# Performance work log

Hardware: AMD Instinct MI355X
Metric: run time of the kernel (lower is better)

## Reference

```python
import jax, jax.numpy as jnp
import numpy as np


def _ccl_8(mask):
    """Connected-component labeling with 8-connectivity (skimage connectivity=2).

    Iterative min-label propagation over the 8-neighborhood, accelerated with
    pointer jumping (label compression), run to convergence via lax.while_loop.
    Returns int32 labels: 0 for background, root_pixel_index+1 for each
    component (equivalent to skimage's labels up to a relabeling permutation).
    """
    H, W = mask.shape
    N = H * W
    BIG = jnp.int32(N)  # background sentinel, also maps to itself in the flat table
    idx = jnp.arange(N, dtype=jnp.int32).reshape(H, W)
    init = jnp.where(mask, idx, BIG)

    def neighbor_min(lab):
        # min over self + 8 neighbors, padded with the BIG sentinel
        p = jnp.pad(lab, 1, constant_values=N)
        m = lab
        for dy in (0, 1, 2):
            for dx in (0, 1, 2):
                m = jnp.minimum(m, p[dy:dy + H, dx:dx + W])
        return jnp.where(mask, m, BIG)

    sentinel = jnp.full((1,), N, dtype=jnp.int32)

    def body(state):
        lab, _ = state
        new = neighbor_min(lab)
        # pointer jumping: hop labels through the label table twice (hop doubling)
        for _ in range(2):
            flat = jnp.concatenate([new.reshape(-1), sentinel])  # [N+1]
            new = flat[new]
        return new, jnp.any(new != lab)

    def cond(state):
        return state[1]

    lab, _ = jax.lax.while_loop(cond, body, (init, jnp.array(True)))
    return jnp.where(mask, lab + 1, 0).astype(jnp.int32)


def setup_inputs() -> dict:
    key = jax.random.key(0)
    prob = jax.random.uniform(key, (1, 1, 2048, 2048), dtype=jnp.float32)
    return {"prob": prob}


def reference(prob):
    # binary_image = (prob > 0.5); squeeze to [H, W]; 8-connected labeling
    mask = (prob > 0.5).reshape(prob.shape[-2], prob.shape[-1])
    return _ccl_8(mask)
```

## Files before the change

### kernel.cpp

```cpp
#include <hip/hip_runtime.h>


#define H 2048
#define W 2048
#define NPIX (H * W)
#define TSX 128
#define TSY 64
#define RPT 4


__device__ __forceinline__ int gfind(int* __restrict__ L, int a) {
    int n = L[a];
    while (n != a + 1) {
        int p = n - 1;
        int g = L[p];
        if (g != n) atomicMin(&L[a], g);
        a = p; n = g;
    }
    return a;
}

__device__ __forceinline__ void gunite(int* __restrict__ L, int a, int b) {
    while (true) {
        a = gfind(L, a);
        b = gfind(L, b);
        if (a == b) return;
        if (a > b) { int t = a; a = b; b = t; }
        int old = atomicMin(&L[b], a + 1);
        if (old == b + 1) return;
        b = old - 1;
    }
}

__device__ __forceinline__ int lfind(volatile int* L, int a) {
    int n = L[a];
    while (n != a) { a = n; n = L[a]; }
    return a;
}

__device__ __forceinline__ int lfind_h(int* L, int a) {
    volatile int* Lv = L;
    int n = Lv[a];
    while (n != a) {
        int g = Lv[n];
        if (g != n) atomicMin(&L[a], g);
        a = n; n = g;
    }
    return a;
}

__device__ __forceinline__ void lunite(int* L, int a, int b) {
    while (true) {
        a = lfind_h(L, a);
        b = lfind_h(L, b);
        if (a == b) return;
        if (a > b) { int t = a; a = b; b = t; }
        int old = atomicMin(&L[b], a);
        if (old == b) return;
        b = old;
    }
}

__device__ __forceinline__ int run_start64(unsigned long long m, int p) {
    if (p == 0) return 0;
    unsigned long long below = m << (64 - p);
    return p - __builtin_clzll(~below);
}

__device__ __forceinline__ int run_start128(unsigned long long u0,
                                            unsigned long long u1, int p) {
    if (p >= 64) {
        int s = run_start64(u1, p - 64) + 64;
        if (s == 64 && (u0 >> 63)) s = run_start64(u0, 63);
        return s;
    }
    return run_start64(u0, p);
}

__device__ __forceinline__ int getbit128(unsigned long long u0,
                                         unsigned long long u1, int p) {
    if (p < 0 || p > 127) return 0;
    return (int)((p < 64 ? (u0 >> p) : (u1 >> (p - 64))) & 1ull);
}

__global__ __launch_bounds__(1024)
void k_local(const float* __restrict__ prob, int* __restrict__ lab,
             int* __restrict__ wsv) {
    __shared__ int slab[TSY * TSX];
    __shared__ unsigned long long mrow0[TSY], mrow1[TSY];
    const int x0 = blockIdx.x * TSX, y0 = blockIdx.y * TSY;
    const int lx = threadIdx.x;
    const int ty = threadIdx.y;

    unsigned long long rM0[RPT], rM1[RPT];
    int sA[RPT], sB[RPT];

    #pragma unroll
    for (int k = 0; k < RPT; ++k) {
        int ly = ty * RPT + k;
        const float* rowp = prob + (long)(y0 + ly) * W + x0;
        bool f0 = rowp[lx] > 0.5f;
        bool f1 = rowp[64 + lx] > 0.5f;
        unsigned long long m0 = __ballot(f0);
        unsigned long long m1 = __ballot(f1);
        rM0[k] = m0; rM1[k] = m1;
        int s0 = f0 ? run_start128(m0, m1, lx) : lx;
        int s1 = f1 ? run_start128(m0, m1, 64 + lx) : 64 + lx;
        sA[k] = s0; sB[k] = s1;
        slab[ly * TSX + lx]      = f0 ? ly * TSX + s0 : -1;
        slab[ly * TSX + 64 + lx] = f1 ? ly * TSX + s1 : -1;
        if (lx == 0) { mrow0[ly] = m0; mrow1[ly] = m1; }
    }
    __syncthreads();

    #pragma unroll
    for (int k = 0; k < RPT; ++k) {
        int ly = ty * RPT + k;
        if (ly == 0) continue;
        unsigned long long u0 = mrow0[ly - 1], u1 = mrow1[ly - 1];
        unsigned long long m0 = rM0[k], m1 = rM1[k];
        #pragma unroll
        for (int h = 0; h < 2; ++h) {
            int pos = h * 64 + lx;
            if (!getbit128(m0, m1, pos)) continue;
            int s = h ? sB[k] : sA[k];
            int mylab = ly * TSX + s;
            if (getbit128(u0, u1, pos)) {
                if (pos == s || !getbit128(u0, u1, pos - 1))
                    lunite(slab, mylab, (ly - 1) * TSX + run_start128(u0, u1, pos));
            } else {
                if (pos == s && getbit128(u0, u1, pos - 1))
                    lunite(slab, mylab, (ly - 1) * TSX + run_start128(u0, u1, pos - 1));
                bool isEnd = (pos == 127) || !getbit128(m0, m1, pos + 1);
                if (isEnd && getbit128(u0, u1, pos + 1))
                    lunite(slab, mylab, (ly - 1) * TSX + (pos + 1));
            }
        }
    }
    __syncthreads();

    #pragma unroll
    for (int k = 0; k < RPT; ++k) {
        int ly = ty * RPT + k;
        unsigned long long m0 = rM0[k], m1 = rM1[k];
        if (((m0 >> lx) & 1) && sA[k] == lx) {
            int li = ly * TSX + lx;
            slab[li] = lfind(slab, li);
        }
        if (((m1 >> lx) & 1) && sB[k] == 64 + lx) {
            int li = ly * TSX + 64 + lx;
            slab[li] = lfind(slab, li);
        }
    }
    __syncthreads();

    #pragma unroll
    for (int k = 0; k < RPT; ++k) {
        int ly = ty * RPT + k;
        unsigned long long m0 = rM0[k], m1 = rM1[k];
        int out0 = 0, out1 = 0;
        if ((m0 >> lx) & 1) {
            int r = slab[ly * TSX + sA[k]];
            out0 = (y0 + (r >> 7)) * W + (x0 + (r & 127)) + 1;
        }
        if ((m1 >> lx) & 1) {
            int r = slab[ly * TSX + sB[k]];
            out1 = (y0 + (r >> 7)) * W + (x0 + (r & 127)) + 1;
        }
        lab[(long)(y0 + ly) * W + x0 + lx]      = out0;
        lab[(long)(y0 + ly) * W + x0 + 64 + lx] = out1;
        if (lx == 0 && blockIdx.x > 0)
            wsv[(blockIdx.x - 1) * 4096 + 2048 + (y0 + ly)] = out0;
        if (lx == 63 && blockIdx.x < 15)
            wsv[blockIdx.x * 4096 + (y0 + ly)] = out1;
    }
}

__global__ __launch_bounds__(256)
void k_seam(int* __restrict__ lab, const int* __restrict__ wsv) {
    int gtid = blockIdx.x * blockDim.x + threadIdx.x;
    int task = gtid >> 6;
    int lane = gtid & 63;
    bool vertical = task < 240;
    int t = vertical ? task : task - 240;
    int seam = t >> 4, chunk = t & 15;

    const int* aPtr;
    const int* bPtr;
    int y_h = 0, xb_h = 0;
    if (vertical) {
        int ybase = chunk << 7;
        aPtr = wsv + seam * 4096 + ybase;
        bPtr = wsv + seam * 4096 + 2048 + ybase;
    } else {
        y_h = (seam + 1) << 6;
        xb_h = chunk << 7;
        bPtr = lab + (long)y_h * W + xb_h;
        aPtr = bPtr - W;
    }
    int B0 = bPtr[lane], B1 = bPtr[64 + lane];
    int A0 = aPtr[lane], A1 = aPtr[64 + lane];

    unsigned long long m0 = __ballot(B0 != 0), m1 = __ballot(B1 != 0);
    unsigned long long u0 = __ballot(A0 != 0), u1 = __ballot(A1 != 0);

    #pragma unroll
    for (int h = 0; h < 2; ++h) {
        int pos = (h << 6) | lane;
        if (!getbit128(m0, m1, pos)) continue;
        int myB = h ? B1 : B0;
        int s = run_start128(m0, m1, pos);
        if (getbit128(u0, u1, pos)) {
            if (pos == s || !getbit128(u0, u1, pos - 1)) {
                int tgt = h ? A1 : A0;
                gunite(lab, myB - 1, tgt - 1);
            }
        } else {
            if (pos == s && pos > 0 && getbit128(u0, u1, pos - 1)) {
                gunite(lab, myB - 1, aPtr[pos - 1] - 1);
            }
            bool isEnd = (pos == 127) || !getbit128(m0, m1, pos + 1);
            if (isEnd && pos < 127 && getbit128(u0, u1, pos + 1)) {
                gunite(lab, myB - 1, aPtr[pos + 1] - 1);
            }
        }
    }

    if (!vertical && lane == 0) {
        if (xb_h > 0 && (m0 & 1) && !(u0 & 1)) {
            int tgt = lab[(long)(y_h - 1) * W + xb_h - 1];
            if (tgt) gunite(lab, B0 - 1, tgt - 1);
        }
        if (xb_h + 128 < W && ((m1 >> 63) & 1) && !((u1 >> 63) & 1)) {
            int tgt = lab[(long)(y_h - 1) * W + xb_h + 128];
            if (tgt) {
                int b127 = lab[(long)y_h * W + xb_h + 127];
                gunite(lab, b127 - 1, tgt - 1);
            }
        }
    }
}

__global__ __launch_bounds__(256)
void k_compress(int* __restrict__ lab) {
    int i = blockIdx.x * blockDim.x + threadIdx.x;
    if (i >= NPIX) return;
    int v = lab[i];
    if (v == 0) return;
    int a = v - 1;
    int n = lab[a];
    while (n != a + 1) { a = n - 1; n = lab[a]; }
    if (a + 1 != v) lab[i] = a + 1;
}

extern "C" void kernel_launch(void* const* d_in, const int* in_sizes, int n_in,
                              void* d_out, int out_size, void* d_ws, size_t ws_size,
                              hipStream_t stream) {
    const float* prob = (const float*)d_in[0];
    int* lab = (int*)d_out;
    int* wsv = (int*)d_ws;

    dim3 lgrid(W / TSX, H / TSY);
    dim3 lblock(64, 16);
    k_local<<<lgrid, lblock, 0, stream>>>(prob, lab, wsv);

    k_seam<<<184, 256, 0, stream>>>(lab, wsv);

    k_compress<<<NPIX / 256, 256, 0, stream>>>(lab);
}
```

Measured before the change: 75.72 us.

## Pre-link runs to first overlapping run, skip redundant unions, vectorize compress

Adds a pass in the local kernel where each run's head pixel writes a direct parent link to the first overlapping run in the row above. The merge pass then skips that already-established union, so fewer atomic lunite calls are made. Local root finding now uses the path-halving find instead of the plain walk. The final compress kernel handles four pixels per thread with int4 loads and stores and reuses the resolved label when adjacent values match. The cost is an extra __syncthreads and pass, plus more per-thread work in compress.

```diff
diff --git a/kernel.cpp b/kernel.cpp
--- a/kernel.cpp
+++ b/kernel.cpp
@@ -32,12 +32,6 @@
     }
 }
 
-__device__ __forceinline__ int lfind(volatile int* L, int a) {
-    int n = L[a];
-    while (n != a) { a = n; n = L[a]; }
-    return a;
-}
-
 __device__ __forceinline__ int lfind_h(int* L, int a) {
     volatile int* Lv = L;
     int n = Lv[a];
@@ -81,6 +75,16 @@
                                          unsigned long long u1, int p) {
     if (p < 0 || p > 127) return 0;
     return (int)((p < 64 ? (u0 >> p) : (u1 >> (p - 64))) & 1ull);
+}
+
+__device__ __forceinline__ int ctz128_from(unsigned long long u0,
+                                           unsigned long long u1, int s) {
+    unsigned long long lo, hi;
+    if (s == 0)      { lo = u0; hi = u1; }
+    else if (s < 64) { lo = (u0 >> s) | (u1 << (64 - s)); hi = u1 >> s; }
+    else             { lo = u1 >> (s - 64); hi = 0; }
+    int t = lo ? __builtin_ctzll(lo) : (hi ? 64 + __builtin_ctzll(hi) : 128);
+    return s + t;
 }
 
 __global__ __launch_bounds__(1024)
@@ -117,6 +121,26 @@
     for (int k = 0; k < RPT; ++k) {
         int ly = ty * RPT + k;
         if (ly == 0) continue;
+        unsigned long long m0 = rM0[k], m1 = rM1[k];
+        unsigned long long u0 = mrow0[ly - 1], u1 = mrow1[ly - 1];
+        #pragma unroll
+        for (int h = 0; h < 2; ++h) {
+            int pos = h * 64 + lx;
+            int s = h ? sB[k] : sA[k];
+            if (!getbit128(m0, m1, pos) || pos != s) continue;
+            int first = ctz128_from(u0, u1, s);
+            if (first > 127) continue;
+            int e = ctz128_from(~m0, ~m1, s) - 1;
+            if (first > e) continue;
+            slab[ly * TSX + s] = (ly - 1) * TSX + run_start128(u0, u1, first);
+        }
+    }
+    __syncthreads();
+
+    #pragma unroll
+    for (int k = 0; k < RPT; ++k) {
+        int ly = ty * RPT + k;
+        if (ly == 0) continue;
         unsigned long long u0 = mrow0[ly - 1], u1 = mrow1[ly - 1];
         unsigned long long m0 = rM0[k], m1 = rM1[k];
         #pragma unroll
@@ -126,8 +150,11 @@
             int s = h ? sB[k] : sA[k];
             int mylab = ly * TSX + s;
             if (getbit128(u0, u1, pos)) {
-                if (pos == s || !getbit128(u0, u1, pos - 1))
-                    lunite(slab, mylab, (ly - 1) * TSX + run_start128(u0, u1, pos));
+                if (pos == s || !getbit128(u0, u1, pos - 1)) {
+                    int first = ctz128_from(u0, u1, s);
+                    if (pos != first)
+                        lunite(slab, mylab, (ly - 1) * TSX + run_start128(u0, u1, pos));
+                }
             } else {
                 if (pos == s && getbit128(u0, u1, pos - 1))
                     lunite(slab, mylab, (ly - 1) * TSX + run_start128(u0, u1, pos - 1));
@@ -145,11 +172,11 @@
         unsigned long long m0 = rM0[k], m1 = rM1[k];
         if (((m0 >> lx) & 1) && sA[k] == lx) {
             int li = ly * TSX + lx;
-            slab[li] = lfind(slab, li);
+            slab[li] = lfind_h(slab, li);
         }
         if (((m1 >> lx) & 1) && sB[k] == 64 + lx) {
             int li = ly * TSX + 64 + lx;
-            slab[li] = lfind(slab, li);
+            slab[li] = lfind_h(slab, li);
         }
     }
     __syncthreads();
@@ -241,16 +268,24 @@
     }
 }
 
+__device__ __forceinline__ int resolve(const int* __restrict__ L, int v) {
+    if (v == 0) return 0;
+    int a = v - 1;
+    int n = L[a];
+    while (n != a + 1) { a = n - 1; n = L[a]; }
+    return a + 1;
+}
+
 __global__ __launch_bounds__(256)
 void k_compress(int* __restrict__ lab) {
-    int i = blockIdx.x * blockDim.x + threadIdx.x;
-    if (i >= NPIX) return;
-    int v = lab[i];
-    if (v == 0) return;
-    int a = v - 1;
-    int n = lab[a];
-    while (n != a + 1) { a = n - 1; n = lab[a]; }
-    if (a + 1 != v) lab[i] = a + 1;
+    int q = blockIdx.x * blockDim.x + threadIdx.x;
+    int4 v = ((const int4*)lab)[q];
+    int o0 = resolve(lab, v.x);
+    int o1 = (v.y == v.x) ? o0 : resolve(lab, v.y);
+    int o2 = (v.z == v.y) ? o1 : resolve(lab, v.z);
+    int o3 = (v.w == v.z) ? o2 : resolve(lab, v.w);
+    if (o0 != v.x || o1 != v.y || o2 != v.z || o3 != v.w)
+        ((int4*)lab)[q] = make_int4(o0, o1, o2, o3);
 }
 
 extern "C" void kernel_launch(void* const* d_in, const int* in_sizes, int n_in,
@@ -266,5 +301,5 @@
 
     k_seam<<<184, 256, 0, stream>>>(lab, wsv);
 
-    k_compress<<<NPIX / 256, 256, 0, stream>>>(lab);
-}
+    k_compress<<<NPIX / 4 / 256, 256, 0, stream>>>(lab);
+}
```

Result: slower. 104.7 us (+38.3%).
